# Optimization experiments

Measured on AMD Instinct MI355X. Metric: run time of the kernel, lower is better.

## Reference

```python
import jax, jax.numpy as jnp
import numpy as np

B = 16384      # batch
F = 512        # input_size (features); n_sites = F + 1, output site at index F//2
D = 16         # bond_dim
P = 2          # physical dim (embedding_dim, poly degree 1 -> [1, x])
OUT = 8        # MPS out_dim (hard-coded in module)
HID = 24       # dense hidden (hard-coded)
NOISE = 0.03


def _interior(key, n):
    # (n, D, P, D) tensors, ~identity on the x^0 slice ('randn_eye'-style init)
    k1, k2 = jax.random.split(key)
    eye = jnp.eye(D, dtype=jnp.float32)
    p0 = eye[None] + NOISE * jax.random.normal(k1, (n, D, D), jnp.float32)
    p1 = NOISE * jax.random.normal(k2, (n, D, D), jnp.float32)
    return jnp.stack([p0, p1], axis=2)


def setup_inputs() -> dict:
    key = jax.random.key(0)
    ks = jax.random.split(key, 9)
    x = jax.random.uniform(ks[0], (B, F), jnp.float32)
    nside = F // 2 - 1  # 255 interior tensors per side
    W_left = _interior(ks[1], nside)          # sites 1 .. F//2-1
    W_right = _interior(ks[2], nside)         # sites F//2+1 .. F-1
    W0 = jnp.eye(P, D, dtype=jnp.float32) + NOISE * jax.random.normal(ks[3], (P, D), jnp.float32)   # left boundary (phys, bond)
    WN = jnp.eye(D, P, dtype=jnp.float32) + NOISE * jax.random.normal(ks[4], (D, P), jnp.float32)   # right boundary (bond, phys)
    W_out = jax.random.normal(ks[5], (D, OUT, D), jnp.float32) / D                                  # output site (bond, out, bond)
    d1_w = 0.3 * jax.random.normal(ks[6], (HID, OUT), jnp.float32)
    d1_b = jnp.zeros((HID,), jnp.float32)
    d2_w = 0.3 * jax.random.normal(ks[7], (1, HID), jnp.float32)
    d2_b = jnp.zeros((1,), jnp.float32)
    return {"x": x, "W0": W0, "W_left": W_left, "W_out": W_out,
            "W_right": W_right, "WN": WN,
            "d1_w": d1_w, "d1_b": d1_b, "d2_w": d2_w, "d2_b": d2_b}


def reference(x, W0, W_left, W_out, W_right, WN, d1_w, d1_b, d2_w, d2_b):
    # poly embedding, degree 1: [x^0, x^1]  -> (B, F, P)
    emb = jnp.stack([jnp.ones_like(x), x], axis=-1)
    half = F // 2

    # ---- left half of the MPS chain: sites 0 .. half-1 ----
    v = jnp.einsum('bp,pd->bd', emb[:, 0], W0)              # (B, D)
    xs_l = jnp.swapaxes(emb[:, 1:half], 0, 1)               # (half-1, B, P)

    def lstep(v, inp):
        xt, W = inp                                         # (B,P), (D,P,D)
        return jnp.einsum('bd,bp,dpe->be', v, xt, W), None

    v, _ = jax.lax.scan(lstep, v, (xs_l, W_left))

    # ---- right half: sites half+1 .. F, contracted right-to-left ----
    u = jnp.einsum('bp,dp->bd', emb[:, -1], WN)             # (B, D)
    xs_r = jnp.swapaxes(emb[:, half:-1], 0, 1)[::-1]        # reversed site order

    def rstep(u, inp):
        xt, W = inp
        return jnp.einsum('dpe,bp,be->bd', W, xt, u), None

    u, _ = jax.lax.scan(rstep, u, (xs_r, W_right[::-1]))

    # ---- output site contraction: (B, OUT) ----
    h = jnp.einsum('bd,doe,be->bo', v, W_out, u)

    # ---- dense head: Linear(8,24) -> Linear(24,1), no activation ----
    h = h @ d1_w.T + d1_b
    y = h @ d2_w.T + d2_b
    return y
```

## Files before the change

kernel.cpp:

```cpp
#include <hip/hip_runtime.h>
#include <stdint.h>

#define B_N    16384
#define F_N    512
#define NPAIR  128
#define CHUNKP 8
#define NCHUNK (NPAIR/CHUNKP)

typedef float    f32x4  __attribute__((ext_vector_type(4)));
typedef short    s16x4  __attribute__((ext_vector_type(4)));
typedef short    s16x8  __attribute__((ext_vector_type(8)));
typedef _Float16 f16x4  __attribute__((ext_vector_type(4)));

typedef __attribute__((address_space(3))) const unsigned short* lds_cptr;

#define DSR(dst, base, offlit) \
  asm volatile("ds_read_b128 %0, %1 offset:" offlit : "=v"(dst) : "v"(base))

#define WS_SIDE_STRIDE 131072
#define WS_M_F         131072
#define WS_C0_F        131328
#define WS_BYTES_NEEDED ((262656 + 2) * 2)

static __device__ __forceinline__ f32x4 MFMA16F(s16x4 a, s16x4 b, f32x4 c) {
  return __builtin_amdgcn_mfma_f32_16x16x16f16(__builtin_bit_cast(f16x4, a),
                                               __builtin_bit_cast(f16x4, b), c, 0, 0, 0);
}

static __device__ __forceinline__ s16x4 packB(const float* st) {
  f16x4 H = {(_Float16)st[0], (_Float16)st[1], (_Float16)st[2], (_Float16)st[3]};
  return __builtin_bit_cast(s16x4, H);
}

static __device__ __forceinline__ s16x4 lo4(s16x8 v) {
  return __builtin_shufflevector(v, v, 0, 1, 2, 3);
}
static __device__ __forceinline__ s16x4 hi4(s16x8 v) {
  return __builtin_shufflevector(v, v, 4, 5, 6, 7);
}

__global__ __launch_bounds__(256) void mps_prep(
    const float* __restrict__ W0, const float* __restrict__ W_left,
    const float* __restrict__ W_out, const float* __restrict__ W_right,
    const float* __restrict__ WN, const float* __restrict__ d1_w,
    const float* __restrict__ d1_b, const float* __restrict__ d2_w,
    const float* __restrict__ d2_b, unsigned short* __restrict__ ws)
{
  int bid = blockIdx.x;
  if (bid < 256) {
    int side = bid >> 7;
    int pair = bid & 127;
    __shared__ float Wa[512];
    __shared__ float Wb[512];
    __shared__ float Amat[4][256];
    int t = threadIdx.x;
    bool pad_a = (pair == 0);
    const float* base_a = side ? (W_right + (size_t)(255 - 2*pair) * 512)
                               : (W_left  + (size_t)(2*pair - 1) * 512);
    const float* base_b = side ? (W_right + (size_t)(254 - 2*pair) * 512)
                               : (W_left  + (size_t)(2*pair) * 512);
#pragma unroll
    for (int e = t; e < 512; e += 256) {
      float va;
      if (pad_a) { int d = e >> 5, p = (e >> 4) & 1, m = e & 15; va = (p == 0 && d == m) ? 1.f : 0.f; }
      else va = base_a[e];
      Wa[e] = va;
      Wb[e] = base_b[e];
    }
    __syncthreads();
#pragma unroll
    for (int ei = t; ei < 1024; ei += 256) {
      int ij = ei >> 8;
      int i_ = ij >> 1, j_ = ij & 1;
      int rem = ei & 255;
      int m = rem >> 4, k = rem & 15;
      float acc = 0.f;
      if (side == 0) {
#pragma unroll
        for (int tt = 0; tt < 16; ++tt) acc += Wa[k*32 + i_*16 + tt] * Wb[tt*32 + j_*16 + m];
      } else {
#pragma unroll
        for (int tt = 0; tt < 16; ++tt) acc += Wb[m*32 + j_*16 + tt] * Wa[tt*32 + i_*16 + k];
      }
      Amat[ij][m*16 + k] = acc;
    }
    __syncthreads();
    if (t < 128) {
      int rg = t >> 6, l = t & 63;
      int m = l & 15, g4 = (l >> 4) * 4;
      s16x8 v8;
#pragma unroll
      for (int i = 0; i < 4; ++i) {
        int k = g4 + i;
        _Float16 h0 = (_Float16)Amat[rg][m*16 + k];
        _Float16 h1 = (_Float16)Amat[2 + rg][m*16 + k];
        v8[i]     = __builtin_bit_cast(short, h0);
        v8[4 + i] = __builtin_bit_cast(short, h1);
      }
      *reinterpret_cast<s16x8*>(ws + (size_t)side * WS_SIDE_STRIDE
                                   + (size_t)pair * 1024 + rg * 512 + l * 8) = v8;
    }
  } else {
    int t = threadIdx.x;
    int d = t >> 4, e = t & 15;
    float acc = 0.f;
#pragma unroll
    for (int o = 0; o < 8; ++o) {
      float wef = 0.f;
      for (int hh = 0; hh < 24; ++hh) wef += d2_w[hh] * d1_w[hh*8 + o];
      acc += wef * W_out[d*128 + o*16 + e];
    }
    float* wf = reinterpret_cast<float*>(ws);
    wf[WS_M_F + t] = acc;
    if (t == 0) {
      float c0 = d2_b[0];
      for (int hh = 0; hh < 24; ++hh) c0 += d2_w[hh] * d1_b[hh];
      wf[WS_C0_F] = c0;
    }
  }
}

__global__ __launch_bounds__(512, 2) void mps_main(
    const float* __restrict__ x, const float* __restrict__ W0,
    const float* __restrict__ WN, const unsigned short* __restrict__ ws,
    float* __restrict__ out)
{
  __shared__ __align__(16) unsigned short sbuf[2][2][CHUNKP][2][64][8];
  __shared__ float fin[2][64][16];

  const int tidx = threadIdx.x;
  const int wave = tidx >> 6;
  const int lane = tidx & 63;
  const int side = wave >> 2;
  const int q    = wave & 3;
  const int n    = lane & 15;
  const int g    = lane >> 4;
  const int b    = blockIdx.x * 64 + q * 16 + n;
  const float* xrow = x + (size_t)b * F_N;

  s16x4 Bv;
  float st[4];
  {
    float xi0 = side ? xrow[F_N-1] : xrow[0];
#pragma unroll
    for (int i = 0; i < 4; ++i) {
      int j = g*4 + i;
      float a0 = side ? WN[j*2]   : W0[j];
      float a1 = side ? WN[j*2+1] : W0[16+j];
      st[i] = fmaf(xi0, a1, a0);
    }
    Bv = packB(st);
  }

  f32x4 Dz = {0.f, 0.f, 0.f, 0.f};

  auto stage = [&](int chunk, int db) {
#pragma unroll
    for (int s2 = 0; s2 < 4; ++s2) {
      int seg = wave * 4 + s2;
      int ss  = seg >> 4;
      int rem = seg & 15;
      int pr  = rem >> 1, fg = rem & 1;
      const unsigned short* src = ws + (size_t)ss * WS_SIDE_STRIDE
                                + (size_t)(chunk * CHUNKP + pr) * 1024 + fg * 512 + lane * 8;
      __builtin_amdgcn_global_load_lds(
        (const __attribute__((address_space(1))) void*)src,
        (__attribute__((address_space(3))) void*)(&sbuf[ss][db][pr][fg][0][0]),
        16, 0, 0);
    }
  };

  auto xbase = [&](int c) { return xrow + (side ? (496 - 16*c) : (16*c)); };

  float4 xq0, xq1, xq2, xq3;
  {
    const float* xp = xbase(0);
    xq0 = *reinterpret_cast<const float4*>(xp);
    xq1 = *reinterpret_cast<const float4*>(xp + 4);
    xq2 = *reinterpret_cast<const float4*>(xp + 8);
    xq3 = *reinterpret_cast<const float4*>(xp + 12);
  }

  stage(0, 0);
  asm volatile("s_waitcnt vmcnt(0)" ::: "memory");
  __syncthreads();

#pragma unroll 1
  for (int c = 0; c < NCHUNK; ++c) {
    float4 xn0 = xq0, xn1 = xq1, xn2 = xq2, xn3 = xq3;
    if (c + 1 < NCHUNK) {
      stage(c + 1, (c + 1) & 1);
      const float* xp = xbase(c + 1);
      xn0 = *reinterpret_cast<const float4*>(xp);
      xn1 = *reinterpret_cast<const float4*>(xp + 4);
      xn2 = *reinterpret_cast<const float4*>(xp + 8);
      xn3 = *reinterpret_cast<const float4*>(xp + 12);
    }

    float xa[8], xb[8];
    {
      float e0=xq0.x, e1=xq0.y, e2=xq0.z, e3=xq0.w, e4=xq1.x, e5=xq1.y, e6=xq1.z, e7=xq1.w;
      float e8=xq2.x, e9=xq2.y, e10=xq2.z, e11=xq2.w, e12=xq3.x, e13=xq3.y, e14=xq3.z, e15=xq3.w;
      if (side == 0) {
        xa[0]=e0;  xb[0]=e1;  xa[1]=e2;  xb[1]=e3;
        xa[2]=e4;  xb[2]=e5;  xa[3]=e6;  xb[3]=e7;
        xa[4]=e8;  xb[4]=e9;  xa[5]=e10; xb[5]=e11;
        xa[6]=e12; xb[6]=e13; xa[7]=e14; xb[7]=e15;
      } else {
        xa[0]=e15; xb[0]=e14; xa[1]=e13; xb[1]=e12;
        xa[2]=e11; xb[2]=e10; xa[3]=e9;  xb[3]=e8;
        xa[4]=e7;  xb[4]=e6;  xa[5]=e5;  xb[5]=e4;
        xa[6]=e3;  xb[6]=e2;  xa[7]=e1;  xb[7]=e0;
      }
    }

    lds_cptr base = (lds_cptr)(&sbuf[side][c & 1][0][0][0][0]) + (size_t)lane * 8;

    s16x8 rA0, rA1, rB0, rB1, rC0, rC1, rD0, rD1;
    DSR(rA0, base, "0");    DSR(rA1, base, "1024");
    {
      lds_cptr bp = base + 1024;
      DSR(rB0, bp, "0");    DSR(rB1, bp, "1024");
    }

#define PAIR_BODY(Rc0, Rc1, Wn0, Wn1, PR, ISSUE, WL)                                    \
  {                                                                                     \
    if (ISSUE) {                                                                        \
      lds_cptr bp = base + (PR + 2) * 1024;                                             \
      DSR(Wn0, bp, "0");                                                                \
      DSR(Wn1, bp, "1024");                                                             \
    }                                                                                   \
    asm volatile("s_waitcnt lgkmcnt(" WL ")" ::: "memory");                             \
    __builtin_amdgcn_sched_barrier(0);                                                  \
    s16x4 a00 = lo4(Rc0), a10 = hi4(Rc0);                                               \
    s16x4 a01 = lo4(Rc1), a11 = hi4(Rc1);                                               \
    f32x4 D00 = MFMA16F(a00, Bv, Dz);                                                   \
    f32x4 D10 = MFMA16F(a10, Bv, Dz);                                                   \
    f32x4 D01 = MFMA16F(a01, Bv, Dz);                                                   \
    f32x4 D11 = MFMA16F(a11, Bv, Dz);                                                   \
    _Pragma("unroll")                                                                   \
    for (int r = 0; r < 4; ++r) {                                                       \
      float t0 = fmaf(xa[PR], D10[r], D00[r]);                                          \
      float t1 = fmaf(xa[PR], D11[r], D01[r]);                                          \
      st[r] = fmaf(xb[PR], t1, t0);                                                     \
    }                                                                                   \
    Bv = packB(st);                                                                     \
  }

    PAIR_BODY(rA0, rA1, rC0, rC1, 0, 1, "4");
    PAIR_BODY(rB0, rB1, rD0, rD1, 1, 1, "4");
    PAIR_BODY(rC0, rC1, rA0, rA1, 2, 1, "4");
    PAIR_BODY(rD0, rD1, rB0, rB1, 3, 1, "4");
    PAIR_BODY(rA0, rA1, rC0, rC1, 4, 1, "4");
    PAIR_BODY(rB0, rB1, rD0, rD1, 5, 1, "4");
    PAIR_BODY(rC0, rC1, rA0, rA1, 6, 0, "2");
    PAIR_BODY(rD0, rD1, rA0, rA1, 7, 0, "0");
#undef PAIR_BODY

    asm volatile("s_waitcnt vmcnt(0)" ::: "memory");
    __syncthreads();
    xq0 = xn0; xq1 = xn1; xq2 = xn2; xq3 = xn3;
  }

#pragma unroll
  for (int r = 0; r < 4; ++r) fin[side][q*16 + n][g*4 + r] = st[r];
  __syncthreads();

  {
    int s = tidx >> 3, j = tidx & 7;
    const float* Mf = reinterpret_cast<const float*>(ws) + WS_M_F;
    float c0 = reinterpret_cast<const float*>(ws)[WS_C0_F];
    float acc = 0.f;
#pragma unroll
    for (int dd = 0; dd < 2; ++dd) {
      int d = j*2 + dd;
      float zd = 0.f;
#pragma unroll
      for (int e = 0; e < 16; ++e) zd = fmaf(Mf[d*16 + e], fin[1][s][e], zd);
      acc = fmaf(fin[0][s][d], zd, acc);
    }
    acc += __shfl_xor(acc, 1, 64);
    acc += __shfl_xor(acc, 2, 64);
    acc += __shfl_xor(acc, 4, 64);
    if (j == 0) out[blockIdx.x*64 + s] = acc + c0;
  }
}

extern "C" void kernel_launch(void* const* d_in, const int* in_sizes, int n_in,
                              void* d_out, int out_size, void* d_ws, size_t ws_size,
                              hipStream_t stream)
{
  const float* x       = (const float*)d_in[0];
  const float* W0      = (const float*)d_in[1];
  const float* W_left  = (const float*)d_in[2];
  const float* W_out   = (const float*)d_in[3];
  const float* W_right = (const float*)d_in[4];
  const float* WN      = (const float*)d_in[5];
  const float* d1_w    = (const float*)d_in[6];
  const float* d1_b    = (const float*)d_in[7];
  const float* d2_w    = (const float*)d_in[8];
  const float* d2_b    = (const float*)d_in[9];
  unsigned short* ws   = (unsigned short*)d_ws;
  float* out           = (float*)d_out;

  if (ws_size < (size_t)WS_BYTES_NEEDED) return;

  hipLaunchKernelGGL(mps_prep, dim3(257), dim3(256), 0, stream,
                     W0, W_left, W_out, W_right, WN, d1_w, d1_b, d2_w, d2_b, ws);
  hipLaunchKernelGGL(mps_main, dim3(B_N/64), dim3(512), 0, stream,
                     x, W0, WN, ws, out);
}
```

Measured before the change: 43.22 us.

## Split left/right MPS chains into separate blocks with a separate head kernel

The fused kernel, where each 512-thread block ran both chain halves for 64 samples, is split in two. A new 256-thread kernel runs one side per block across 512 blocks and writes its final 16-float bond vector to the workspace. A new head kernel then contracts v, M and u per sample. This is meant to raise occupancy and scheduling flexibility through smaller blocks and halved LDS per block. In exchange it adds an extra kernel launch and a global round-trip of 2x16384x16 floats.

```diff
diff --git a/kernel.cpp b/kernel.cpp
--- a/kernel.cpp
+++ b/kernel.cpp
@@ -20,7 +20,9 @@
 #define WS_SIDE_STRIDE 131072
 #define WS_M_F         131072
 #define WS_C0_F        131328
-#define WS_BYTES_NEEDED ((262656 + 2) * 2)
+#define WS_VU_F        131344
+#define WS_U_OFF       262144
+#define WS_BYTES_NEEDED ((size_t)(WS_VU_F + 2*262144) * 4)
 
 static __device__ __forceinline__ f32x4 MFMA16F(s16x4 a, s16x4 b, f32x4 c) {
   return __builtin_amdgcn_mfma_f32_16x16x16f16(__builtin_bit_cast(f16x4, a),
@@ -120,22 +122,21 @@
   }
 }
 
-__global__ __launch_bounds__(512, 2) void mps_main(
+__global__ __launch_bounds__(256, 2) void mps_side(
     const float* __restrict__ x, const float* __restrict__ W0,
-    const float* __restrict__ WN, const unsigned short* __restrict__ ws,
-    float* __restrict__ out)
+    const float* __restrict__ WN, unsigned short* __restrict__ ws)
 {
-  __shared__ __align__(16) unsigned short sbuf[2][2][CHUNKP][2][64][8];
-  __shared__ float fin[2][64][16];
+  __shared__ __align__(16) unsigned short sbuf[2][CHUNKP][2][64][8];
 
   const int tidx = threadIdx.x;
   const int wave = tidx >> 6;
   const int lane = tidx & 63;
-  const int side = wave >> 2;
-  const int q    = wave & 3;
+  const int bid  = blockIdx.x;
+  const int side = bid >> 8;
+  const int sb   = bid & 255;
   const int n    = lane & 15;
   const int g    = lane >> 4;
-  const int b    = blockIdx.x * 64 + q * 16 + n;
+  const int b    = sb * 64 + wave * 16 + n;
   const float* xrow = x + (size_t)b * F_N;
 
   s16x4 Bv;
@@ -158,14 +159,12 @@
 #pragma unroll
     for (int s2 = 0; s2 < 4; ++s2) {
       int seg = wave * 4 + s2;
-      int ss  = seg >> 4;
-      int rem = seg & 15;
-      int pr  = rem >> 1, fg = rem & 1;
-      const unsigned short* src = ws + (size_t)ss * WS_SIDE_STRIDE
+      int pr  = seg >> 1, fg = seg & 1;
+      const unsigned short* src = ws + (size_t)side * WS_SIDE_STRIDE
                                 + (size_t)(chunk * CHUNKP + pr) * 1024 + fg * 512 + lane * 8;
       __builtin_amdgcn_global_load_lds(
         (const __attribute__((address_space(1))) void*)src,
-        (__attribute__((address_space(3))) void*)(&sbuf[ss][db][pr][fg][0][0]),
+        (__attribute__((address_space(3))) void*)(&sbuf[db][pr][fg][0][0]),
         16, 0, 0);
     }
   };
@@ -214,7 +213,7 @@
       }
     }
 
-    lds_cptr base = (lds_cptr)(&sbuf[side][c & 1][0][0][0][0]) + (size_t)lane * 8;
+    lds_cptr base = (lds_cptr)(&sbuf[c & 1][0][0][0][0]) + (size_t)lane * 8;
 
     s16x8 rA0, rA1, rB0, rB1, rC0, rC1, rD0, rD1;
     DSR(rA0, base, "0");    DSR(rA1, base, "1024");
@@ -262,28 +261,45 @@
     xq0 = xn0; xq1 = xn1; xq2 = xn2; xq3 = xn3;
   }
 
-#pragma unroll
-  for (int r = 0; r < 4; ++r) fin[side][q*16 + n][g*4 + r] = st[r];
+  {
+    float* vu = reinterpret_cast<float*>(ws) + WS_VU_F
+              + (size_t)side * WS_U_OFF + (size_t)b * 16 + g * 4;
+    float4 o = {st[0], st[1], st[2], st[3]};
+    *reinterpret_cast<float4*>(vu) = o;
+  }
+}
+
+__global__ __launch_bounds__(256) void mps_head(
+    const unsigned short* __restrict__ ws, float* __restrict__ out)
+{
+  __shared__ float Msh[256];
+  __shared__ float c0s;
+  const float* wf = reinterpret_cast<const float*>(ws);
+  int t = threadIdx.x;
+  Msh[t] = wf[WS_M_F + t];
+  if (t == 0) c0s = wf[WS_C0_F];
   __syncthreads();
 
-  {
-    int s = tidx >> 3, j = tidx & 7;
-    const float* Mf = reinterpret_cast<const float*>(ws) + WS_M_F;
-    float c0 = reinterpret_cast<const float*>(ws)[WS_C0_F];
-    float acc = 0.f;
-#pragma unroll
-    for (int dd = 0; dd < 2; ++dd) {
-      int d = j*2 + dd;
-      float zd = 0.f;
-#pragma unroll
-      for (int e = 0; e < 16; ++e) zd = fmaf(Mf[d*16 + e], fin[1][s][e], zd);
-      acc = fmaf(fin[0][s][d], zd, acc);
-    }
-    acc += __shfl_xor(acc, 1, 64);
-    acc += __shfl_xor(acc, 2, 64);
-    acc += __shfl_xor(acc, 4, 64);
-    if (j == 0) out[blockIdx.x*64 + s] = acc + c0;
-  }
+  int s = blockIdx.x * 256 + t;
+  const float* vp = wf + WS_VU_F + (size_t)s * 16;
+  const float* up = wf + WS_VU_F + WS_U_OFF + (size_t)s * 16;
+  float v[16], u[16];
+#pragma unroll
+  for (int i = 0; i < 4; ++i) {
+    float4 a = *reinterpret_cast<const float4*>(vp + i*4);
+    float4 c = *reinterpret_cast<const float4*>(up + i*4);
+    v[i*4+0]=a.x; v[i*4+1]=a.y; v[i*4+2]=a.z; v[i*4+3]=a.w;
+    u[i*4+0]=c.x; u[i*4+1]=c.y; u[i*4+2]=c.z; u[i*4+3]=c.w;
+  }
+  float acc = 0.f;
+#pragma unroll
+  for (int d = 0; d < 16; ++d) {
+    float zd = 0.f;
+#pragma unroll
+    for (int e = 0; e < 16; ++e) zd = fmaf(Msh[d*16 + e], u[e], zd);
+    acc = fmaf(v[d], zd, acc);
+  }
+  out[s] = acc + c0s;
 }
 
 extern "C" void kernel_launch(void* const* d_in, const int* in_sizes, int n_in,
@@ -303,10 +319,12 @@
   unsigned short* ws   = (unsigned short*)d_ws;
   float* out           = (float*)d_out;
 
-  if (ws_size < (size_t)WS_BYTES_NEEDED) return;
+  if (ws_size < WS_BYTES_NEEDED) return;
 
   hipLaunchKernelGGL(mps_prep, dim3(257), dim3(256), 0, stream,
                      W0, W_left, W_out, W_right, WN, d1_w, d1_b, d2_w, d2_b, ws);
-  hipLaunchKernelGGL(mps_main, dim3(B_N/64), dim3(512), 0, stream,
-                     x, W0, WN, ws, out);
-}
+  hipLaunchKernelGGL(mps_side, dim3(512), dim3(256), 0, stream,
+                     x, W0, WN, ws);
+  hipLaunchKernelGGL(mps_head, dim3(B_N/256), dim3(256), 0, stream,
+                     ws, out);
+}
```

After: 38.40 us. -11.2%, faster.
